# Kernel tuning notes

Hardware: AMD Instinct MI355X
Metric: run time of the kernel (lower is better)

## Reference

```python
import jax, jax.numpy as jnp
import numpy as np

B, S, E, H = 4, 2048, 256, 8
D = E // H
SCALE = D ** -0.5


def setup_inputs() -> dict:
    key = jax.random.key(0)
    k1, k2, k3, k4, k5, k6 = jax.random.split(key, 6)
    x = jax.random.normal(k1, (B, S, E), dtype=jnp.float32)
    lengths = jax.random.randint(k2, (B,), S // 4, S + 1)
    # binary prefix mask, as assumed by mask[i].sum() == valid length in the original
    mask = (jnp.arange(S)[None, :] < lengths[:, None]).astype(jnp.int32)
    w_std = 1.0 / np.sqrt(E)
    Wq = jax.random.normal(k3, (E, E), dtype=jnp.float32) * w_std
    Wk = jax.random.normal(k4, (E, E), dtype=jnp.float32) * w_std
    Wv = jax.random.normal(k5, (E, E), dtype=jnp.float32) * w_std
    Wo = jax.random.normal(k6, (E, E), dtype=jnp.float32) * w_std
    return {"x": x, "mask": mask, "Wq": Wq, "Wk": Wk, "Wv": Wv, "Wo": Wo}


def _scramble_pad(attn_i, L):
    # attn_i: [S, H, D] attention output for one sample; only query rows < L are used.
    # Faithful to torch: attn[:L] viewed as [H, L, D] (after transpose(1,2)) then
    # reshape(L, E), zero-padded to [S, E]. The reshape mixes heads in a
    # length-dependent way, reproduced here with integer index arithmetic.
    L_safe = jnp.maximum(L, 1)
    flat = jnp.arange(S * E)                     # flat index into [H, L, D] row-major
    h = jnp.minimum(flat // (L_safe * D), H - 1)
    rem = flat % (L_safe * D)
    s = rem // D
    d = rem % D
    valid = flat < L * E
    vals = attn_i[s, h, d]
    return jnp.where(valid, vals, 0.0).reshape(S, E)


def reference(x, mask, Wq, Wk, Wv, Wo):
    # projections (torch Linear, no bias: y = x @ W.T), split heads
    Q = (x @ Wq.T).reshape(B, S, H, D)
    K = (x @ Wk.T).reshape(B, S, H, D)
    V = (x @ Wv.T).reshape(B, S, H, D)
    scores = jnp.einsum("bqhd,bkhd->bhqk", Q, K) * SCALE
    key_valid = mask[:, None, None, :] > 0       # prefix key mask == per-sample varlen attn
    scores = jnp.where(key_valid, scores, -1e30)
    P = jax.nn.softmax(scores, axis=-1)
    attn = jnp.einsum("bhqk,bkhd->bqhd", P, V)   # [B, S, H, D]
    lengths = mask.sum(axis=1)
    padded = jax.vmap(_scramble_pad)(attn, lengths)  # [B, S, E]
    return padded @ Wo.T
```

## Files before the change

### kernel.cpp

```cpp
#include <hip/hip_runtime.h>
#include <cmath>

#define Bn 4
#define Sn 2048
#define En 256
#define Hn 8
#define Dn 32
#define KD 256
#define NS 4
#define CHUNK 512

static constexpr float SCALE_LOG2E = 0.25504210472155044f;

typedef _Float16 half4_t __attribute__((ext_vector_type(4)));
typedef _Float16 half8_t __attribute__((ext_vector_type(8)));
typedef float float4_t __attribute__((ext_vector_type(4)));

__global__ __launch_bounds__(256) void cvt_kernel(
    const float* __restrict__ Wq, const float* __restrict__ Wk,
    const float* __restrict__ Wv, const float* __restrict__ Wo,
    const int* __restrict__ mask, _Float16* __restrict__ Wh,
    int* __restrict__ len) {
  if (blockIdx.x == 128) {
    const int b = threadIdx.x >> 6, lane = threadIdx.x & 63;
    int s = 0;
    for (int i = lane; i < Sn; i += 64) s += mask[b * Sn + i];
#pragma unroll
    for (int off = 32; off > 0; off >>= 1) s += __shfl_down(s, off, 64);
    if (lane == 0) len[b] = s;
    return;
  }
  const size_t wi = ((size_t)blockIdx.x * 256 + threadIdx.x) * 8;
  const int w = (int)(wi >> 16);
  const size_t off = wi & 65535;
  const float* src = (w == 0) ? Wq : (w == 1) ? Wk : (w == 2) ? Wv : Wo;
  float4 a = *(const float4*)&src[off];
  float4 b2 = *(const float4*)&src[off + 4];
  half8_t h;
  h[0] = (_Float16)a.x;  h[1] = (_Float16)a.y;
  h[2] = (_Float16)a.z;  h[3] = (_Float16)a.w;
  h[4] = (_Float16)b2.x; h[5] = (_Float16)b2.y;
  h[6] = (_Float16)b2.z; h[7] = (_Float16)b2.w;
  *(half8_t*)&(Wh + (size_t)w * 65536)[off] = h;
}

__global__ __launch_bounds__(256) void qkv_gemm(
    const float* __restrict__ x, const _Float16* __restrict__ Wh,
    _Float16* __restrict__ Qh, _Float16* __restrict__ Kh,
    _Float16* __restrict__ Vt) {
  const int lane = threadIdx.x & 63;
  const int wv = threadIdx.x >> 6;
  const int quad = lane >> 4, l15 = lane & 15;
  const int fid = blockIdx.x + 12 * blockIdx.y;
  const int wl = (fid & 7) * 48 + (fid >> 3);
  const int nb = wl % 12, mb = wl / 12;
  const int n0 = nb * 64;
  const int mw = mb * 256 + wv * 64;

  float4_t C[4][4];
#pragma unroll
  for (int i = 0; i < 4; ++i)
#pragma unroll
    for (int j = 0; j < 4; ++j) C[i][j] = (float4_t){0.f, 0.f, 0.f, 0.f};

  for (int k0 = 0; k0 < KD; k0 += 32) {
    half8_t A[4], Bf[4];
#pragma unroll
    for (int i = 0; i < 4; ++i) {
      const float4* xp =
          (const float4*)&x[(size_t)(mw + 16 * i + l15) * KD + k0 + quad * 8];
      const float4 a0 = xp[0], a1 = xp[1];
      A[i][0] = (_Float16)a0.x; A[i][1] = (_Float16)a0.y;
      A[i][2] = (_Float16)a0.z; A[i][3] = (_Float16)a0.w;
      A[i][4] = (_Float16)a1.x; A[i][5] = (_Float16)a1.y;
      A[i][6] = (_Float16)a1.z; A[i][7] = (_Float16)a1.w;
    }
#pragma unroll
    for (int j = 0; j < 4; ++j)
      Bf[j] = *(const half8_t*)&Wh[(size_t)(n0 + 16 * j + l15) * KD + k0 + quad * 8];
#pragma unroll
    for (int i = 0; i < 4; ++i)
#pragma unroll
      for (int j = 0; j < 4; ++j)
        C[i][j] = __builtin_amdgcn_mfma_f32_16x16x32_f16(A[i], Bf[j], C[i][j], 0, 0, 0);
  }

  const int mat = n0 >> 8;
  if (mat < 2) {
    _Float16* dstH = mat ? Kh : Qh;
    const float scale = mat ? 1.0f : SCALE_LOG2E;
#pragma unroll
    for (int i = 0; i < 4; ++i)
#pragma unroll
      for (int j = 0; j < 4; ++j) {
        const int c = ((n0 + 16 * j) & 255) + l15;
        const int h = c >> 5, d = c & 31;
#pragma unroll
        for (int r = 0; r < 4; ++r) {
          const int m = mw + 16 * i + quad * 4 + r;
          const int b = m >> 11, s = m & (Sn - 1);
          dstH[((size_t)(b * Hn + h) * Sn + s) * Dn + d] =
              (_Float16)(C[i][j][r] * scale);
        }
      }
  } else {
#pragma unroll
    for (int i = 0; i < 4; ++i)
#pragma unroll
      for (int j = 0; j < 4; ++j) {
        const int c = ((n0 + 16 * j) & 255) + l15;
        const int h = c >> 5, d = c & 31;
        const int m = mw + 16 * i + quad * 4;
        const int b = m >> 11, s = m & (Sn - 1);
        half4_t hv;
#pragma unroll
        for (int r = 0; r < 4; ++r) hv[r] = (_Float16)C[i][j][r];
        *(half4_t*)&Vt[(size_t)(b * Hn + h) * (Sn * Dn) +
                       (size_t)(s >> 5) * 1024 + d * 32 + (s & 31)] = hv;
      }
  }
}

__global__ __launch_bounds__(256) void out_gemm(
    const _Float16* __restrict__ Ph, const _Float16* __restrict__ Woh,
    float* __restrict__ out) {
  const int lane = threadIdx.x & 63;
  const int wv = threadIdx.x >> 6;
  const int quad = lane >> 4, l15 = lane & 15;
  const int fid = blockIdx.x + 4 * blockIdx.y;
  const int wl = (fid & 7) * 16 + (fid >> 3);
  const int nb = wl % 4, mb = wl / 4;
  const int n0 = nb * 64;
  const int mw = mb * 256 + wv * 64;

  float4_t C[4][4];
#pragma unroll
  for (int i = 0; i < 4; ++i)
#pragma unroll
    for (int j = 0; j < 4; ++j) C[i][j] = (float4_t){0.f, 0.f, 0.f, 0.f};

  for (int k0 = 0; k0 < KD; k0 += 32) {
    half8_t A[4], Bf[4];
#pragma unroll
    for (int i = 0; i < 4; ++i)
      A[i] = *(const half8_t*)&Ph[(size_t)(mw + 16 * i + l15) * KD + k0 + quad * 8];
#pragma unroll
    for (int j = 0; j < 4; ++j)
      Bf[j] = *(const half8_t*)&Woh[(size_t)(n0 + 16 * j + l15) * KD + k0 + quad * 8];
#pragma unroll
    for (int i = 0; i < 4; ++i)
#pragma unroll
      for (int j = 0; j < 4; ++j)
        C[i][j] = __builtin_amdgcn_mfma_f32_16x16x32_f16(A[i], Bf[j], C[i][j], 0, 0, 0);
  }

#pragma unroll
  for (int i = 0; i < 4; ++i)
#pragma unroll
    for (int j = 0; j < 4; ++j)
#pragma unroll
      for (int r = 0; r < 4; ++r)
        out[(size_t)(mw + 16 * i + quad * 4 + r) * En + n0 + 16 * j + l15] =
            C[i][j][r];
}

__global__ __launch_bounds__(256) void attn_kernel(
    const _Float16* __restrict__ Qh, const _Float16* __restrict__ Kh,
    const _Float16* __restrict__ Vt, const int* __restrict__ len,
    _Float16* __restrict__ pacc, float* __restrict__ pl) {
  const int lid = blockIdx.x + 64 * (blockIdx.y + 8 * blockIdx.z);
  const int h = lid & 7;
  const int rest = lid >> 3;
  const int b = rest >> 6;
  const int inner = rest & 63;
  const int split = inner & (NS - 1);
  const int qg = inner >> 2;

  const int L = len[b];
  const int lane = threadIdx.x & 63;
  const int wv = threadIdx.x >> 6;
  const int q0 = (qg * 4 + wv) * 32;
  if (q0 >= L) return;
  const int ks = split * CHUNK;
  if (ks >= L) return;
  const int ke = min(L, ks + CHUNK);

  const int quad = lane >> 4;
  const int l15 = lane & 15;
  const size_t bh = (size_t)(b * Hn + h) * Sn;
  const _Float16* Vt0 = &Vt[(size_t)(b * Hn + h) * (Sn * Dn)];

  half8_t qf[2];
#pragma unroll
  for (int t = 0; t < 2; ++t)
    qf[t] = *(const half8_t*)&Qh[(bh + q0 + 16 * t + l15) * Dn + quad * 8];

  float4_t o0[2], o1[2];
  float ll[2];
#pragma unroll
  for (int t = 0; t < 2; ++t) {
    o0[t] = (float4_t){0.f, 0.f, 0.f, 0.f};
    o1[t] = (float4_t){0.f, 0.f, 0.f, 0.f};
    ll[t] = 0.f;
  }

  const int vo0 = l15 * 32 + quad * 4;
  const int vo1 = (l15 + 16) * 32 + quad * 4;

  const _Float16* vt_c = &Vt0[(size_t)(ks >> 5) * 1024];
  half8_t kfc0 = *(const half8_t*)&Kh[(bh + ks + l15) * Dn + quad * 8];
  half8_t kfc1 = *(const half8_t*)&Kh[(bh + ks + 16 + l15) * Dn + quad * 8];
  half4_t v0c = *(const half4_t*)&vt_c[vo0];
  half4_t v1c = *(const half4_t*)&vt_c[vo1];
  half4_t v2c = *(const half4_t*)&vt_c[vo0 + 16];
  half4_t v3c = *(const half4_t*)&vt_c[vo1 + 16];

  for (int k0 = ks; k0 < ke; k0 += 32) {
    const int kn = (k0 + 32 < ke) ? k0 + 32 : ks;
    const _Float16* vt_n = &Vt0[(size_t)(kn >> 5) * 1024];
    const half8_t kfn0 = *(const half8_t*)&Kh[(bh + kn + l15) * Dn + quad * 8];
    const half8_t kfn1 = *(const half8_t*)&Kh[(bh + kn + 16 + l15) * Dn + quad * 8];
    const half4_t v0n = *(const half4_t*)&vt_n[vo0];
    const half4_t v1n = *(const half4_t*)&vt_n[vo1];
    const half4_t v2n = *(const half4_t*)&vt_n[vo0 + 16];
    const half4_t v3n = *(const half4_t*)&vt_n[vo1 + 16];

    float4_t st0[2], st1[2];
#pragma unroll
    for (int t = 0; t < 2; ++t) {
      st0[t] = (float4_t){0.f, 0.f, 0.f, 0.f};
      st1[t] = (float4_t){0.f, 0.f, 0.f, 0.f};
      st0[t] = __builtin_amdgcn_mfma_f32_16x16x32_f16(kfc0, qf[t], st0[t], 0, 0, 0);
      st1[t] = __builtin_amdgcn_mfma_f32_16x16x32_f16(kfc1, qf[t], st1[t], 0, 0, 0);
    }

    if (k0 + 32 <= ke) {
#pragma unroll
      for (int t = 0; t < 2; ++t) {
        half4_t pf0, pf1;
#pragma unroll
        for (int r = 0; r < 4; ++r) {
          const float pa = __builtin_amdgcn_exp2f(st0[t][r]);
          const float pb = __builtin_amdgcn_exp2f(st1[t][r]);
          ll[t] += pa + pb;
          pf0[r] = (_Float16)pa;
          pf1[r] = (_Float16)pb;
        }
        o0[t] = __builtin_amdgcn_mfma_f32_16x16x16f16(pf0, v0c, o0[t], 0, 0, 0);
        o1[t] = __builtin_amdgcn_mfma_f32_16x16x16f16(pf0, v1c, o1[t], 0, 0, 0);
        o0[t] = __builtin_amdgcn_mfma_f32_16x16x16f16(pf1, v2c, o0[t], 0, 0, 0);
        o1[t] = __builtin_amdgcn_mfma_f32_16x16x16f16(pf1, v3c, o1[t], 0, 0, 0);
      }
    } else {
      const int ka = k0 + quad * 4, kb = k0 + 16 + quad * 4;
#pragma unroll
      for (int t = 0; t < 2; ++t) {
        half4_t pf0, pf1;
#pragma unroll
        for (int r = 0; r < 4; ++r) {
          const float pa = __builtin_amdgcn_exp2f((ka + r < ke) ? st0[t][r] : -3.0e38f);
          const float pb = __builtin_amdgcn_exp2f((kb + r < ke) ? st1[t][r] : -3.0e38f);
          ll[t] += pa + pb;
          pf0[r] = (_Float16)pa;
          pf1[r] = (_Float16)pb;
        }
        o0[t] = __builtin_amdgcn_mfma_f32_16x16x16f16(pf0, v0c, o0[t], 0, 0, 0);
        o1[t] = __builtin_amdgcn_mfma_f32_16x16x16f16(pf0, v1c, o1[t], 0, 0, 0);
        o0[t] = __builtin_amdgcn_mfma_f32_16x16x16f16(pf1, v2c, o0[t], 0, 0, 0);
        o1[t] = __builtin_amdgcn_mfma_f32_16x16x16f16(pf1, v3c, o1[t], 0, 0, 0);
      }
    }
    kfc0 = kfn0; kfc1 = kfn1;
    v0c = v0n; v1c = v1n; v2c = v2n; v3c = v3n;
  }

#pragma unroll
  for (int t = 0; t < 2; ++t) {
    ll[t] += __shfl_xor(ll[t], 16);
    ll[t] += __shfl_xor(ll[t], 32);
  }

  const size_t idx0 = ((size_t)(b * Hn + h) * NS + split) * Sn + q0;
#pragma unroll
  for (int t = 0; t < 2; ++t) {
#pragma unroll
    for (int r = 0; r < 4; ++r) {
      _Float16* pp = &pacc[(idx0 + 16 * t + quad * 4 + r) * 32];
      pp[l15] = (_Float16)o0[t][r];
      pp[l15 + 16] = (_Float16)o1[t][r];
    }
  }
  if (quad == 0) {
#pragma unroll
    for (int t = 0; t < 2; ++t) pl[idx0 + 16 * t + l15] = ll[t];
  }
}

__global__ __launch_bounds__(256) void combine_kernel(const _Float16* __restrict__ pacc,
                                                      const float* __restrict__ pl,
                                                      const int* __restrict__ len,
                                                      _Float16* __restrict__ Ph) {
  const int b = blockIdx.z;
  const int L = len[b];
  if (blockIdx.y == Hn) {
    _Float16* base = Ph + (size_t)b * Sn * En;
    const size_t end = (size_t)Sn * En;
    const size_t stride = (size_t)gridDim.x * 256 * 8;
    half8_t z = {0, 0, 0, 0, 0, 0, 0, 0};
    for (size_t idx = (size_t)L * En + ((size_t)blockIdx.x * 256 + threadIdx.x) * 8;
         idx < end; idx += stride)
      *(half8_t*)&base[idx] = z;
    return;
  }
  const int h = blockIdx.y;
  const int q = blockIdx.x * 256 + threadIdx.x;
  if (q >= L) return;
  const size_t base = (size_t)(b * Hn + h) * NS * Sn;

  float T = 0.f;
  float o[32];
#pragma unroll
  for (int d = 0; d < 32; ++d) o[d] = 0.f;
#pragma unroll
  for (int sp = 0; sp < NS; ++sp) {
    if (sp * CHUNK < L) {
      T += pl[base + (size_t)sp * Sn + q];
      const half8_t* pp = (const half8_t*)&pacc[(base + (size_t)sp * Sn + q) * 32];
#pragma unroll
      for (int i = 0; i < 4; ++i) {
        half8_t v = pp[i];
#pragma unroll
        for (int t2 = 0; t2 < 8; ++t2) o[i * 8 + t2] += (float)v[t2];
      }
    }
  }
  const float inv = 1.0f / T;
  _Float16* dst = &Ph[(size_t)b * Sn * En + (size_t)h * L * Dn + (size_t)q * Dn];
#pragma unroll
  for (int i = 0; i < 4; ++i) {
    half8_t hv;
#pragma unroll
    for (int t2 = 0; t2 < 8; ++t2) hv[t2] = (_Float16)(o[i * 8 + t2] * inv);
    *(half8_t*)&dst[i * 8] = hv;
  }
}

extern "C" void kernel_launch(void* const* d_in, const int* in_sizes, int n_in,
                              void* d_out, int out_size, void* d_ws, size_t ws_size,
                              hipStream_t stream) {
  (void)in_sizes; (void)n_in; (void)out_size; (void)ws_size;
  const float* x  = (const float*)d_in[0];
  const int* mask = (const int*)d_in[1];
  const float* Wq = (const float*)d_in[2];
  const float* Wk = (const float*)d_in[3];
  const float* Wv = (const float*)d_in[4];
  const float* Wo = (const float*)d_in[5];
  float* out = (float*)d_out;

  float* wsf = (float*)d_ws;
  int* lengths = (int*)d_ws;
  const size_t BHSD = (size_t)Bn * Hn * Sn * Dn;
  _Float16* Wh = (_Float16*)(wsf + 64);
  _Float16* Qh = Wh + 4 * 65536;
  _Float16* Kh = Qh + BHSD;
  _Float16* Vt = Kh + BHSD;
  _Float16* Ph = Vt + BHSD;
  _Float16* pacc = Ph + BHSD;
  float* pl = (float*)(pacc + (size_t)Bn * Hn * NS * Sn * 32);

  cvt_kernel<<<dim3(129), 256, 0, stream>>>(Wq, Wk, Wv, Wo, mask, Wh, lengths);
  qkv_gemm<<<dim3(12, 32), 256, 0, stream>>>(x, Wh, Qh, Kh, Vt);
  attn_kernel<<<dim3((Sn / 128) * NS, Hn, Bn), 256, 0, stream>>>(
      Qh, Kh, Vt, lengths, pacc, pl);
  combine_kernel<<<dim3(Sn / 256, Hn + 1, Bn), 256, 0, stream>>>(
      pacc, pl, lengths, Ph);
  out_gemm<<<dim3(4, 32), 256, 0, stream>>>(Ph, Wh + 3 * 65536, out);
}
```

Measured before the change: 148.6 us.

## Double query rows per wave, prefetch K/V two steps ahead, raise MFMA priority

Each wave in the attention kernel now handles 64 query rows instead of 32, so each K/V fragment load feeds twice as many MFMAs, and the grid is halved to match. K/V register prefetch is deepened from one to two iterations ahead to hide more global-load latency. s_setprio raises wave priority around the MFMA/exp block. The cost is higher register pressure, which may lower occupancy, and fewer blocks, which gives coarser load balance over variable-length sequences.

Measured after the change: 143.4 us. -3.5%, faster.

```diff
diff --git a/kernel.cpp b/kernel.cpp
--- a/kernel.cpp
+++ b/kernel.cpp
@@ -168,18 +168,18 @@
     const _Float16* __restrict__ Qh, const _Float16* __restrict__ Kh,
     const _Float16* __restrict__ Vt, const int* __restrict__ len,
     _Float16* __restrict__ pacc, float* __restrict__ pl) {
-  const int lid = blockIdx.x + 64 * (blockIdx.y + 8 * blockIdx.z);
+  const int lid = blockIdx.x + 32 * (blockIdx.y + 8 * blockIdx.z);
   const int h = lid & 7;
-  const int rest = lid >> 3;
-  const int b = rest >> 6;
-  const int inner = rest & 63;
+  const int w = lid >> 3;
+  const int b = w >> 5;
+  const int inner = w & 31;
   const int split = inner & (NS - 1);
   const int qg = inner >> 2;
 
   const int L = len[b];
   const int lane = threadIdx.x & 63;
   const int wv = threadIdx.x >> 6;
-  const int q0 = (qg * 4 + wv) * 32;
+  const int q0 = (qg * 4 + wv) * 64;
   if (q0 >= L) return;
   const int ks = split * CHUNK;
   if (ks >= L) return;
@@ -190,15 +190,15 @@
   const size_t bh = (size_t)(b * Hn + h) * Sn;
   const _Float16* Vt0 = &Vt[(size_t)(b * Hn + h) * (Sn * Dn)];
 
-  half8_t qf[2];
-#pragma unroll
-  for (int t = 0; t < 2; ++t)
+  half8_t qf[4];
+#pragma unroll
+  for (int t = 0; t < 4; ++t)
     qf[t] = *(const half8_t*)&Qh[(bh + q0 + 16 * t + l15) * Dn + quad * 8];
 
-  float4_t o0[2], o1[2];
-  float ll[2];
-#pragma unroll
-  for (int t = 0; t < 2; ++t) {
+  float4_t o0[4], o1[4];
+  float ll[4];
+#pragma unroll
+  for (int t = 0; t < 4; ++t) {
     o0[t] = (float4_t){0.f, 0.f, 0.f, 0.f};
     o1[t] = (float4_t){0.f, 0.f, 0.f, 0.f};
     ll[t] = 0.f;
@@ -215,19 +215,30 @@
   half4_t v2c = *(const half4_t*)&vt_c[vo0 + 16];
   half4_t v3c = *(const half4_t*)&vt_c[vo1 + 16];
 
+  const int r1 = (ks + 32 < ke) ? ks + 32 : ks;
+  const _Float16* vt_1 = &Vt0[(size_t)(r1 >> 5) * 1024];
+  half8_t kfn0 = *(const half8_t*)&Kh[(bh + r1 + l15) * Dn + quad * 8];
+  half8_t kfn1 = *(const half8_t*)&Kh[(bh + r1 + 16 + l15) * Dn + quad * 8];
+  half4_t v0n = *(const half4_t*)&vt_1[vo0];
+  half4_t v1n = *(const half4_t*)&vt_1[vo1];
+  half4_t v2n = *(const half4_t*)&vt_1[vo0 + 16];
+  half4_t v3n = *(const half4_t*)&vt_1[vo1 + 16];
+
   for (int k0 = ks; k0 < ke; k0 += 32) {
-    const int kn = (k0 + 32 < ke) ? k0 + 32 : ks;
-    const _Float16* vt_n = &Vt0[(size_t)(kn >> 5) * 1024];
-    const half8_t kfn0 = *(const half8_t*)&Kh[(bh + kn + l15) * Dn + quad * 8];
-    const half8_t kfn1 = *(const half8_t*)&Kh[(bh + kn + 16 + l15) * Dn + quad * 8];
-    const half4_t v0n = *(const half4_t*)&vt_n[vo0];
-    const half4_t v1n = *(const half4_t*)&vt_n[vo1];
-    const half4_t v2n = *(const half4_t*)&vt_n[vo0 + 16];
-    const half4_t v3n = *(const half4_t*)&vt_n[vo1 + 16];
-
-    float4_t st0[2], st1[2];
-#pragma unroll
-    for (int t = 0; t < 2; ++t) {
+    const int kp = k0 + 64;
+    const int kn = (kp < ke) ? kp : ks;
+    const _Float16* vt_t = &Vt0[(size_t)(kn >> 5) * 1024];
+    const half8_t kft0 = *(const half8_t*)&Kh[(bh + kn + l15) * Dn + quad * 8];
+    const half8_t kft1 = *(const half8_t*)&Kh[(bh + kn + 16 + l15) * Dn + quad * 8];
+    const half4_t v0t = *(const half4_t*)&vt_t[vo0];
+    const half4_t v1t = *(const half4_t*)&vt_t[vo1];
+    const half4_t v2t = *(const half4_t*)&vt_t[vo0 + 16];
+    const half4_t v3t = *(const half4_t*)&vt_t[vo1 + 16];
+
+    __builtin_amdgcn_s_setprio(1);
+    float4_t st0[4], st1[4];
+#pragma unroll
+    for (int t = 0; t < 4; ++t) {
       st0[t] = (float4_t){0.f, 0.f, 0.f, 0.f};
       st1[t] = (float4_t){0.f, 0.f, 0.f, 0.f};
       st0[t] = __builtin_amdgcn_mfma_f32_16x16x32_f16(kfc0, qf[t], st0[t], 0, 0, 0);
@@ -236,7 +247,7 @@
 
     if (k0 + 32 <= ke) {
 #pragma unroll
-      for (int t = 0; t < 2; ++t) {
+      for (int t = 0; t < 4; ++t) {
         half4_t pf0, pf1;
 #pragma unroll
         for (int r = 0; r < 4; ++r) {
@@ -254,7 +265,7 @@
     } else {
       const int ka = k0 + quad * 4, kb = k0 + 16 + quad * 4;
 #pragma unroll
-      for (int t = 0; t < 2; ++t) {
+      for (int t = 0; t < 4; ++t) {
         half4_t pf0, pf1;
 #pragma unroll
         for (int r = 0; r < 4; ++r) {
@@ -270,19 +281,22 @@
         o1[t] = __builtin_amdgcn_mfma_f32_16x16x16f16(pf1, v3c, o1[t], 0, 0, 0);
       }
     }
+    __builtin_amdgcn_s_setprio(0);
     kfc0 = kfn0; kfc1 = kfn1;
     v0c = v0n; v1c = v1n; v2c = v2n; v3c = v3n;
-  }
-
-#pragma unroll
-  for (int t = 0; t < 2; ++t) {
+    kfn0 = kft0; kfn1 = kft1;
+    v0n = v0t; v1n = v1t; v2n = v2t; v3n = v3t;
+  }
+
+#pragma unroll
+  for (int t = 0; t < 4; ++t) {
     ll[t] += __shfl_xor(ll[t], 16);
     ll[t] += __shfl_xor(ll[t], 32);
   }
 
   const size_t idx0 = ((size_t)(b * Hn + h) * NS + split) * Sn + q0;
 #pragma unroll
-  for (int t = 0; t < 2; ++t) {
+  for (int t = 0; t < 4; ++t) {
 #pragma unroll
     for (int r = 0; r < 4; ++r) {
       _Float16* pp = &pacc[(idx0 + 16 * t + quad * 4 + r) * 32];
@@ -292,7 +306,7 @@
   }
   if (quad == 0) {
 #pragma unroll
-    for (int t = 0; t < 2; ++t) pl[idx0 + 16 * t + l15] = ll[t];
+    for (int t = 0; t < 4; ++t) pl[idx0 + 16 * t + l15] = ll[t];
   }
 }
 
@@ -370,7 +384,7 @@
 
   cvt_kernel<<<dim3(129), 256, 0, stream>>>(Wq, Wk, Wv, Wo, mask, Wh, lengths);
   qkv_gemm<<<dim3(12, 32), 256, 0, stream>>>(x, Wh, Qh, Kh, Vt);
-  attn_kernel<<<dim3((Sn / 128) * NS, Hn, Bn), 256, 0, stream>>>(
+  attn_kernel<<<dim3((Sn / 256) * NS, Hn, Bn), 256, 0, stream>>>(
       Qh, Kh, Vt, lengths, pacc, pl);
   combine_kernel<<<dim3(Sn / 256, Hn + 1, Bn), 256, 0, stream>>>(
       pacc, pl, lengths, Ph);
```

## Drop split-K attention and combine kernel; single-wave blocks cover full key range

Applied to the files above, without the earlier changes.

Replaces the split-K attention (four key chunks written to partial buffers, then a separate combine kernel) with one 64-thread wave per block that processes 64 queries over the whole key range and normalises in registers. Zero-padding of the rows past the valid length moves into the attention kernel. This removes a kernel launch and the partial-result global write and read traffic. In exchange each wave does more sequential work and there are fewer waves in flight overall, which may reduce latency hiding on long sequences.

Result: faster. 143.3 us (-3.5%).

```diff
diff --git a/kernel.cpp b/kernel.cpp
--- a/kernel.cpp
+++ b/kernel.cpp
@@ -7,8 +7,6 @@
 #define Hn 8
 #define Dn 32
 #define KD 256
-#define NS 4
-#define CHUNK 512
 
 static constexpr float SCALE_LOG2E = 0.25504210472155044f;
 
@@ -164,184 +162,141 @@
             C[i][j][r];
 }
 
-__global__ __launch_bounds__(256) void attn_kernel(
+__global__ __launch_bounds__(64) void attn_kernel(
     const _Float16* __restrict__ Qh, const _Float16* __restrict__ Kh,
     const _Float16* __restrict__ Vt, const int* __restrict__ len,
-    _Float16* __restrict__ pacc, float* __restrict__ pl) {
-  const int lid = blockIdx.x + 64 * (blockIdx.y + 8 * blockIdx.z);
-  const int h = lid & 7;
-  const int rest = lid >> 3;
-  const int b = rest >> 6;
-  const int inner = rest & 63;
-  const int split = inner & (NS - 1);
-  const int qg = inner >> 2;
-
-  const int L = len[b];
-  const int lane = threadIdx.x & 63;
-  const int wv = threadIdx.x >> 6;
-  const int q0 = (qg * 4 + wv) * 32;
-  if (q0 >= L) return;
-  const int ks = split * CHUNK;
-  if (ks >= L) return;
-  const int ke = min(L, ks + CHUNK);
-
-  const int quad = lane >> 4;
-  const int l15 = lane & 15;
-  const size_t bh = (size_t)(b * Hn + h) * Sn;
-  const _Float16* Vt0 = &Vt[(size_t)(b * Hn + h) * (Sn * Dn)];
-
-  half8_t qf[2];
-#pragma unroll
-  for (int t = 0; t < 2; ++t)
-    qf[t] = *(const half8_t*)&Qh[(bh + q0 + 16 * t + l15) * Dn + quad * 8];
-
-  float4_t o0[2], o1[2];
-  float ll[2];
-#pragma unroll
-  for (int t = 0; t < 2; ++t) {
-    o0[t] = (float4_t){0.f, 0.f, 0.f, 0.f};
-    o1[t] = (float4_t){0.f, 0.f, 0.f, 0.f};
-    ll[t] = 0.f;
-  }
-
-  const int vo0 = l15 * 32 + quad * 4;
-  const int vo1 = (l15 + 16) * 32 + quad * 4;
-
-  const _Float16* vt_c = &Vt0[(size_t)(ks >> 5) * 1024];
-  half8_t kfc0 = *(const half8_t*)&Kh[(bh + ks + l15) * Dn + quad * 8];
-  half8_t kfc1 = *(const half8_t*)&Kh[(bh + ks + 16 + l15) * Dn + quad * 8];
-  half4_t v0c = *(const half4_t*)&vt_c[vo0];
-  half4_t v1c = *(const half4_t*)&vt_c[vo1];
-  half4_t v2c = *(const half4_t*)&vt_c[vo0 + 16];
-  half4_t v3c = *(const half4_t*)&vt_c[vo1 + 16];
-
-  for (int k0 = ks; k0 < ke; k0 += 32) {
-    const int kn = (k0 + 32 < ke) ? k0 + 32 : ks;
-    const _Float16* vt_n = &Vt0[(size_t)(kn >> 5) * 1024];
-    const half8_t kfn0 = *(const half8_t*)&Kh[(bh + kn + l15) * Dn + quad * 8];
-    const half8_t kfn1 = *(const half8_t*)&Kh[(bh + kn + 16 + l15) * Dn + quad * 8];
-    const half4_t v0n = *(const half4_t*)&vt_n[vo0];
-    const half4_t v1n = *(const half4_t*)&vt_n[vo1];
-    const half4_t v2n = *(const half4_t*)&vt_n[vo0 + 16];
-    const half4_t v3n = *(const half4_t*)&vt_n[vo1 + 16];
-
-    float4_t st0[2], st1[2];
-#pragma unroll
-    for (int t = 0; t < 2; ++t) {
-      st0[t] = (float4_t){0.f, 0.f, 0.f, 0.f};
-      st1[t] = (float4_t){0.f, 0.f, 0.f, 0.f};
-      st0[t] = __builtin_amdgcn_mfma_f32_16x16x32_f16(kfc0, qf[t], st0[t], 0, 0, 0);
-      st1[t] = __builtin_amdgcn_mfma_f32_16x16x32_f16(kfc1, qf[t], st1[t], 0, 0, 0);
-    }
-
-    if (k0 + 32 <= ke) {
-#pragma unroll
-      for (int t = 0; t < 2; ++t) {
-        half4_t pf0, pf1;
-#pragma unroll
-        for (int r = 0; r < 4; ++r) {
-          const float pa = __builtin_amdgcn_exp2f(st0[t][r]);
-          const float pb = __builtin_amdgcn_exp2f(st1[t][r]);
-          ll[t] += pa + pb;
-          pf0[r] = (_Float16)pa;
-          pf1[r] = (_Float16)pb;
-        }
-        o0[t] = __builtin_amdgcn_mfma_f32_16x16x16f16(pf0, v0c, o0[t], 0, 0, 0);
-        o1[t] = __builtin_amdgcn_mfma_f32_16x16x16f16(pf0, v1c, o1[t], 0, 0, 0);
-        o0[t] = __builtin_amdgcn_mfma_f32_16x16x16f16(pf1, v2c, o0[t], 0, 0, 0);
-        o1[t] = __builtin_amdgcn_mfma_f32_16x16x16f16(pf1, v3c, o1[t], 0, 0, 0);
-      }
-    } else {
-      const int ka = k0 + quad * 4, kb = k0 + 16 + quad * 4;
-#pragma unroll
-      for (int t = 0; t < 2; ++t) {
-        half4_t pf0, pf1;
-#pragma unroll
-        for (int r = 0; r < 4; ++r) {
-          const float pa = __builtin_amdgcn_exp2f((ka + r < ke) ? st0[t][r] : -3.0e38f);
-          const float pb = __builtin_amdgcn_exp2f((kb + r < ke) ? st1[t][r] : -3.0e38f);
-          ll[t] += pa + pb;
-          pf0[r] = (_Float16)pa;
-          pf1[r] = (_Float16)pb;
-        }
-        o0[t] = __builtin_amdgcn_mfma_f32_16x16x16f16(pf0, v0c, o0[t], 0, 0, 0);
-        o1[t] = __builtin_amdgcn_mfma_f32_16x16x16f16(pf0, v1c, o1[t], 0, 0, 0);
-        o0[t] = __builtin_amdgcn_mfma_f32_16x16x16f16(pf1, v2c, o0[t], 0, 0, 0);
-        o1[t] = __builtin_amdgcn_mfma_f32_16x16x16f16(pf1, v3c, o1[t], 0, 0, 0);
-      }
-    }
-    kfc0 = kfn0; kfc1 = kfn1;
-    v0c = v0n; v1c = v1n; v2c = v2n; v3c = v3n;
-  }
-
-#pragma unroll
-  for (int t = 0; t < 2; ++t) {
-    ll[t] += __shfl_xor(ll[t], 16);
-    ll[t] += __shfl_xor(ll[t], 32);
-  }
-
-  const size_t idx0 = ((size_t)(b * Hn + h) * NS + split) * Sn + q0;
-#pragma unroll
-  for (int t = 0; t < 2; ++t) {
-#pragma unroll
-    for (int r = 0; r < 4; ++r) {
-      _Float16* pp = &pacc[(idx0 + 16 * t + quad * 4 + r) * 32];
-      pp[l15] = (_Float16)o0[t][r];
-      pp[l15 + 16] = (_Float16)o1[t][r];
-    }
-  }
-  if (quad == 0) {
-#pragma unroll
-    for (int t = 0; t < 2; ++t) pl[idx0 + 16 * t + l15] = ll[t];
-  }
-}
-
-__global__ __launch_bounds__(256) void combine_kernel(const _Float16* __restrict__ pacc,
-                                                      const float* __restrict__ pl,
-                                                      const int* __restrict__ len,
-                                                      _Float16* __restrict__ Ph) {
+    _Float16* __restrict__ Ph) {
+  const int h = blockIdx.x;
+  const int qg = blockIdx.y;
   const int b = blockIdx.z;
   const int L = len[b];
-  if (blockIdx.y == Hn) {
-    _Float16* base = Ph + (size_t)b * Sn * En;
-    const size_t end = (size_t)Sn * En;
-    const size_t stride = (size_t)gridDim.x * 256 * 8;
+  const int q0 = qg * 64;
+  const int lane = threadIdx.x;
+  const int quad = lane >> 4, l15 = lane & 15;
+
+  _Float16* Phb = Ph + (size_t)b * Sn * En;
+
+  if (q0 < L) {
+    const int ke = L;
+    const size_t bh = (size_t)(b * Hn + h) * Sn;
+    const _Float16* Vt0 = &Vt[(size_t)(b * Hn + h) * (Sn * Dn)];
+
+    half8_t qf[4];
+#pragma unroll
+    for (int t = 0; t < 4; ++t)
+      qf[t] = *(const half8_t*)&Qh[(bh + q0 + 16 * t + l15) * Dn + quad * 8];
+
+    float4_t o0[4], o1[4];
+    float ll[4];
+#pragma unroll
+    for (int t = 0; t < 4; ++t) {
+      o0[t] = (float4_t){0.f, 0.f, 0.f, 0.f};
+      o1[t] = (float4_t){0.f, 0.f, 0.f, 0.f};
+      ll[t] = 0.f;
+    }
+
+    const int vo0 = l15 * 32 + quad * 4;
+    const int vo1 = (l15 + 16) * 32 + quad * 4;
+
+    const _Float16* vt_c = Vt0;
+    half8_t kfc0 = *(const half8_t*)&Kh[(bh + l15) * Dn + quad * 8];
+    half8_t kfc1 = *(const half8_t*)&Kh[(bh + 16 + l15) * Dn + quad * 8];
+    half4_t v0c = *(const half4_t*)&vt_c[vo0];
+    half4_t v1c = *(const half4_t*)&vt_c[vo1];
+    half4_t v2c = *(const half4_t*)&vt_c[vo0 + 16];
+    half4_t v3c = *(const half4_t*)&vt_c[vo1 + 16];
+
+    for (int k0 = 0; k0 < ke; k0 += 32) {
+      const int kn = (k0 + 32 < ke) ? k0 + 32 : 0;
+      const _Float16* vt_n = &Vt0[(size_t)(kn >> 5) * 1024];
+      const half8_t kfn0 = *(const half8_t*)&Kh[(bh + kn + l15) * Dn + quad * 8];
+      const half8_t kfn1 = *(const half8_t*)&Kh[(bh + kn + 16 + l15) * Dn + quad * 8];
+      const half4_t v0n = *(const half4_t*)&vt_n[vo0];
+      const half4_t v1n = *(const half4_t*)&vt_n[vo1];
+      const half4_t v2n = *(const half4_t*)&vt_n[vo0 + 16];
+      const half4_t v3n = *(const half4_t*)&vt_n[vo1 + 16];
+
+      float4_t st0[4], st1[4];
+#pragma unroll
+      for (int t = 0; t < 4; ++t) {
+        st0[t] = (float4_t){0.f, 0.f, 0.f, 0.f};
+        st1[t] = (float4_t){0.f, 0.f, 0.f, 0.f};
+        st0[t] = __builtin_amdgcn_mfma_f32_16x16x32_f16(kfc0, qf[t], st0[t], 0, 0, 0);
+        st1[t] = __builtin_amdgcn_mfma_f32_16x16x32_f16(kfc1, qf[t], st1[t], 0, 0, 0);
+      }
+
+      if (k0 + 32 <= ke) {
+#pragma unroll
+        for (int t = 0; t < 4; ++t) {
+          half4_t pf0, pf1;
+#pragma unroll
+          for (int r = 0; r < 4; ++r) {
+            const float pa = __builtin_amdgcn_exp2f(st0[t][r]);
+            const float pb = __builtin_amdgcn_exp2f(st1[t][r]);
+            ll[t] += pa + pb;
+            pf0[r] = (_Float16)pa;
+            pf1[r] = (_Float16)pb;
+          }
+          o0[t] = __builtin_amdgcn_mfma_f32_16x16x16f16(pf0, v0c, o0[t], 0, 0, 0);
+          o1[t] = __builtin_amdgcn_mfma_f32_16x16x16f16(pf0, v1c, o1[t], 0, 0, 0);
+          o0[t] = __builtin_amdgcn_mfma_f32_16x16x16f16(pf1, v2c, o0[t], 0, 0, 0);
+          o1[t] = __builtin_amdgcn_mfma_f32_16x16x16f16(pf1, v3c, o1[t], 0, 0, 0);
+        }
+      } else {
+        const int ka = k0 + quad * 4, kb = k0 + 16 + quad * 4;
+#pragma unroll
+        for (int t = 0; t < 4; ++t) {
+          half4_t pf0, pf1;
+#pragma unroll
+          for (int r = 0; r < 4; ++r) {
+            const float pa = __builtin_amdgcn_exp2f((ka + r < ke) ? st0[t][r] : -3.0e38f);
+            const float pb = __builtin_amdgcn_exp2f((kb + r < ke) ? st1[t][r] : -3.0e38f);
+            ll[t] += pa + pb;
+            pf0[r] = (_Float16)pa;
+            pf1[r] = (_Float16)pb;
+          }
+          o0[t] = __builtin_amdgcn_mfma_f32_16x16x16f16(pf0, v0c, o0[t], 0, 0, 0);
+          o1[t] = __builtin_amdgcn_mfma_f32_16x16x16f16(pf0, v1c, o1[t], 0, 0, 0);
+          o0[t] = __builtin_amdgcn_mfma_f32_16x16x16f16(pf1, v2c, o0[t], 0, 0, 0);
+          o1[t] = __builtin_amdgcn_mfma_f32_16x16x16f16(pf1, v3c, o1[t], 0, 0, 0);
+        }
+      }
+      kfc0 = kfn0; kfc1 = kfn1;
+      v0c = v0n; v1c = v1n; v2c = v2n; v3c = v3n;
+    }
+
+#pragma unroll
+    for (int t = 0; t < 4; ++t) {
+      ll[t] += __shfl_xor(ll[t], 16);
+      ll[t] += __shfl_xor(ll[t], 32);
+    }
+
+    _Float16* dsth = Phb + (size_t)h * L * Dn;
+#pragma unroll
+    for (int t = 0; t < 4; ++t) {
+      float Tq[4];
+#pragma unroll
+      for (int r = 0; r < 4; ++r)
+        Tq[r] = __shfl(ll[t], (quad << 2) | r);
+#pragma unroll
+      for (int r = 0; r < 4; ++r) {
+        const int q = q0 + 16 * t + (quad << 2) + r;
+        if (q < L) {
+          const float inv = 1.0f / Tq[r];
+          _Float16* dst = dsth + (size_t)q * Dn;
+          dst[l15] = (_Float16)(o0[t][r] * inv);
+          dst[l15 + 16] = (_Float16)(o1[t][r] * inv);
+        }
+      }
+    }
+  }
+
+  if (h == (qg & 7) && q0 + 64 > L) {
+    const int zs = (q0 > L) ? q0 : L;
+    const size_t end = (size_t)(q0 + 64) * En;
     half8_t z = {0, 0, 0, 0, 0, 0, 0, 0};
-    for (size_t idx = (size_t)L * En + ((size_t)blockIdx.x * 256 + threadIdx.x) * 8;
-         idx < end; idx += stride)
-      *(half8_t*)&base[idx] = z;
-    return;
-  }
-  const int h = blockIdx.y;
-  const int q = blockIdx.x * 256 + threadIdx.x;
-  if (q >= L) return;
-  const size_t base = (size_t)(b * Hn + h) * NS * Sn;
-
-  float T = 0.f;
-  float o[32];
-#pragma unroll
-  for (int d = 0; d < 32; ++d) o[d] = 0.f;
-#pragma unroll
-  for (int sp = 0; sp < NS; ++sp) {
-    if (sp * CHUNK < L) {
-      T += pl[base + (size_t)sp * Sn + q];
-      const half8_t* pp = (const half8_t*)&pacc[(base + (size_t)sp * Sn + q) * 32];
-#pragma unroll
-      for (int i = 0; i < 4; ++i) {
-        half8_t v = pp[i];
-#pragma unroll
-        for (int t2 = 0; t2 < 8; ++t2) o[i * 8 + t2] += (float)v[t2];
-      }
-    }
-  }
-  const float inv = 1.0f / T;
-  _Float16* dst = &Ph[(size_t)b * Sn * En + (size_t)h * L * Dn + (size_t)q * Dn];
-#pragma unroll
-  for (int i = 0; i < 4; ++i) {
-    half8_t hv;
-#pragma unroll
-    for (int t2 = 0; t2 < 8; ++t2) hv[t2] = (_Float16)(o[i * 8 + t2] * inv);
-    *(half8_t*)&dst[i * 8] = hv;
+    for (size_t idx = (size_t)zs * En + (size_t)lane * 8; idx < end; idx += 64 * 8)
+      *(half8_t*)&Phb[idx] = z;
   }
 }
 
@@ -365,14 +320,10 @@
   _Float16* Kh = Qh + BHSD;
   _Float16* Vt = Kh + BHSD;
   _Float16* Ph = Vt + BHSD;
-  _Float16* pacc = Ph + BHSD;
-  float* pl = (float*)(pacc + (size_t)Bn * Hn * NS * Sn * 32);
 
   cvt_kernel<<<dim3(129), 256, 0, stream>>>(Wq, Wk, Wv, Wo, mask, Wh, lengths);
   qkv_gemm<<<dim3(12, 32), 256, 0, stream>>>(x, Wh, Qh, Kh, Vt);
-  attn_kernel<<<dim3((Sn / 128) * NS, Hn, Bn), 256, 0, stream>>>(
-      Qh, Kh, Vt, lengths, pacc, pl);
-  combine_kernel<<<dim3(Sn / 256, Hn + 1, Bn), 256, 0, stream>>>(
-      pacc, pl, lengths, Ph);
+  attn_kernel<<<dim3(Hn, Sn / 64, Bn), 64, 0, stream>>>(
+      Qh, Kh, Vt, lengths, Ph);
   out_gemm<<<dim3(4, 32), 256, 0, stream>>>(Ph, Wh + 3 * 65536, out);
 }
```
